# Optimization experiments

Hardware: AMD Instinct MI355X
Metric: run time of the kernel (lower is better)

## Reference

```python
import jax, jax.numpy as jnp
import numpy as np

B, T, I, H, C, S, V = 32, 64, 300, 168, 168, 512, 50257


def setup_inputs() -> dict:
    key = jax.random.key(0)
    ks = jax.random.split(key, 10)
    s = 0.05
    return {
        "x": jax.random.normal(ks[0], (B, T, I), jnp.float32),
        "context": jax.random.normal(ks[1], (B, S, C), jnp.float32),
        "context_lengths": jax.random.randint(ks[2], (B,), 1, S + 1),
        "W_ih": jax.random.normal(ks[3], (4 * H, I + C), jnp.float32) * s,
        "W_hh": jax.random.normal(ks[4], (4 * H, H), jnp.float32) * s,
        "b_ih": jnp.zeros((4 * H,), jnp.float32),
        "b_hh": jnp.zeros((4 * H,), jnp.float32),
        "att_Wx": jax.random.normal(ks[5], (H, H), jnp.float32) * s,
        "att_Ws": jax.random.normal(ks[6], (C, H), jnp.float32) * s,
        "att_b": jnp.zeros((H,), jnp.float32),
        "att_v": jax.random.normal(ks[7], (H,), jnp.float32) * s,
        "W_dec": jax.random.normal(ks[8], (V, H), jnp.float32) * s,
    }


def reference(x, context, context_lengths, W_ih, W_hh, b_ih, b_hh,
              att_Wx, att_Ws, att_b, att_v, W_dec):
    # x: (B, T, I); context: (B, S, C)
    b, t, _ = x.shape
    s_len = context.shape[1]
    h_dim = W_hh.shape[1]
    dtype = x.dtype

    # valid-position mask for attention over source context
    mask = jnp.arange(s_len)[None, :] < context_lengths[:, None]  # (B, S)
    # seq projection is time-invariant: precompute once outside the step loop
    seq_proj = jnp.einsum('bsc,ca->bsa', context, att_Ws)  # (B, S, H)

    h0 = jnp.zeros((b, h_dim), dtype)
    c0 = jnp.zeros((b, h_dim), dtype)

    def step(carry, x_t):
        h, c = carry
        # MLP (additive) attention: v . tanh(Wx h + Ws seq + b)
        e = jnp.einsum('bsa,a->bs',
                       jnp.tanh((h @ att_Wx)[:, None, :] + seq_proj + att_b),
                       att_v)  # (B, S)
        e = jnp.where(mask, e, jnp.asarray(-1e9, dtype))
        w = jax.nn.softmax(e, axis=-1)
        attn_ctx = jnp.einsum('bs,bsc->bc', w, context)  # (B, C)

        # concat input with attended context, single-layer LSTM cell
        rnn_in = jnp.concatenate([x_t, attn_ctx], axis=1)  # (B, I+C)
        gates = rnn_in @ W_ih.T + b_ih + h @ W_hh.T + b_hh  # (B, 4H)
        i_g, f_g, g_g, o_g = jnp.split(gates, 4, axis=1)    # torch ifgo order
        c_new = jax.nn.sigmoid(f_g) * c + jax.nn.sigmoid(i_g) * jnp.tanh(g_g)
        h_new = jax.nn.sigmoid(o_g) * jnp.tanh(c_new)

        dec = h_new @ W_dec.T  # (B, V), bias-free decode
        return (h_new, c_new), dec

    _, decs = jax.lax.scan(step, (h0, c0), jnp.swapaxes(x, 0, 1))  # (T, B, V)
    return jnp.swapaxes(decs, 0, 1)  # (B, T, V)
```

## Files before the change

### kernel.cpp

```cpp
#include <hip/hip_runtime.h>
#include <stdint.h>

#define BB 32
#define TT 64
#define ID 300
#define HH 168
#define SS 512
#define VV 50257
#define G4 672
#define IC 468
#define KP 192
#define NP2 50432
#define NJ 8
#define RPB 21
#define CPB 84
#define KK 336
#define WKP 88
#define EPAD 170
#define SBLK 64
#define LP 72

typedef float f32x4 __attribute__((ext_vector_type(4)));
typedef short bf16x8 __attribute__((ext_vector_type(8)));

__device__ __forceinline__ float bf2f(unsigned short u) {
  union { unsigned int i; float f; } v; v.i = ((unsigned int)u) << 16; return v.f;
}
__device__ __forceinline__ unsigned short f2bf(float f) {
  union { float f; unsigned int u; } v; v.f = f;
  unsigned int r = v.u + 0x7fffu + ((v.u >> 16) & 1u);
  return (unsigned short)(r >> 16);
}
__device__ __forceinline__ float rcpf(float x) { return __builtin_amdgcn_rcpf(x); }

#define NB_WDEC 4728
#define NB_TR   788
__global__ void k_prepall(const float* __restrict__ Wih, const float* __restrict__ Whh,
                          const float* __restrict__ attWx, const float* __restrict__ Wd,
                          float* __restrict__ WihxT, unsigned short* __restrict__ Wdb,
                          float* __restrict__ WgT, unsigned short* __restrict__ WxS,
                          unsigned int* __restrict__ flags, unsigned short* __restrict__ hall) {
  const int bid = blockIdx.x, tid = threadIdx.x;
  if (bid < NB_WDEC) {
    size_t e0 = ((size_t)bid * 256 + tid) * 8;
    int v = (int)(e0 / KP), k = (int)(e0 - (size_t)v * KP);
    unsigned short o[8];
    if (v < VV && k < HH) {
      const float* src = Wd + (size_t)v * HH + k;
      #pragma unroll
      for (int i = 0; i < 8; ++i) o[i] = f2bf(src[i]);
    } else {
      #pragma unroll
      for (int i = 0; i < 8; ++i) o[i] = 0;
    }
    *(uint4*)(Wdb + e0) = *(const uint4*)o;
    return;
  }
  if (bid < NB_WDEC + NB_TR) {
    int idx = (bid - NB_WDEC) * 256 + tid;
    if (idx < ID * G4) {
      int k = idx / G4, i = idx - k * G4;
      WihxT[idx] = Wih[(size_t)i * IC + k];
    }
    return;
  }
  int idx = (bid - NB_WDEC - NB_TR) * 256 + tid;
  const int T1 = NJ * KK * WKP;
  const int T2 = T1 + NJ * RPB * HH;
  const int T3 = T2 + 2 * BB * NJ * 64;
  const int T4 = T3 + BB * TT * (KP - HH);
  if (idx < T1) {
    int j = idx / (KK * WKP); int r = idx - j * (KK * WKP);
    int k = r / WKP, col = r - k * WKP;
    float w = 0.f;
    if (col < CPB) {
      int gt = col / RPB, rr = col - gt * RPB;
      int gcol = gt * HH + j * RPB + rr;
      w = (k < HH) ? Wih[(size_t)gcol * IC + ID + k] : Whh[(size_t)gcol * HH + (k - HH)];
    }
    WgT[idx] = w;
  } else if (idx < T2) {
    int r = idx - T1;
    WxS[r] = f2bf(attWx[r]);
  } else if (idx < T3) {
    flags[idx - T2] = 0u;
  } else if (idx < T4) {
    int r = idx - T3;
    int bt = r / (KP - HH), c = r - bt * (KP - HH);
    hall[(size_t)bt * KP + HH + c] = 0;
  }
}

__global__ void k_seqxp(const float* __restrict__ ctx, const float* __restrict__ Ws,
                        const float* __restrict__ x, const float* __restrict__ WihxT,
                        const float* __restrict__ bih, const float* __restrict__ bhh,
                        unsigned short* __restrict__ ETs, unsigned short* __restrict__ ctxb,
                        float* __restrict__ Xp) {
  __shared__ float sbuf[2688];
  const int tid = threadIdx.x;
  if (blockIdx.x < 1024) {
    const int b = blockIdx.x & 31;
    const int s0 = (blockIdx.x >> 5) * 16;
    for (int idx = tid; idx < 16 * HH; idx += 256) {
      float v = ctx[(size_t)(b * SS + s0) * HH + idx];
      sbuf[idx] = v;
      ctxb[(size_t)(b * SS + s0) * HH + idx] = f2bf(v);
    }
    __syncthreads();
    #pragma unroll
    for (int o = 0; o < 11; ++o) {
      int idx = o * 256 + tid;
      if (idx < 16 * HH) {
        int s = idx / HH, h = idx - s * HH;
        const float* cr = &sbuf[s * HH];
        float acc = 0.f;
        #pragma unroll 4
        for (int c = 0; c < HH; ++c) acc = fmaf(cr[c], Ws[c * HH + h], acc);
        ETs[(size_t)(b * SS + s0 + s) * HH + h] = f2bf(__expf(2.f * acc));
      }
    }
  } else {
    const int r = blockIdx.x - 1024;
    const int t0 = (r & 7) * 8;
    const int b = r >> 3;
    for (int idx = tid; idx < 8 * ID; idx += 256)
      sbuf[idx] = x[(size_t)(b * TT + t0) * ID + idx];
    __syncthreads();
    for (int i = tid; i < G4; i += 256) {
      float bias = bih[i] + bhh[i];
      float acc[8];
      #pragma unroll
      for (int tt = 0; tt < 8; ++tt) acc[tt] = bias;
      for (int k = 0; k < ID; ++k) {
        float w = WihxT[k * G4 + i];
        #pragma unroll
        for (int tt = 0; tt < 8; ++tt) acc[tt] += sbuf[tt * ID + k] * w;
      }
      #pragma unroll
      for (int tt = 0; tt < 8; ++tt)
        Xp[(size_t)(b * TT + t0 + tt) * G4 + i] = acc[tt];
    }
  }
}

__global__ __launch_bounds__(512, 1) void k_recur(
    const int* __restrict__ lens, const float* __restrict__ attb,
    const float* __restrict__ attv, const float* __restrict__ WgT,
    const unsigned short* __restrict__ WxS, const unsigned short* __restrict__ ETs,
    const unsigned short* __restrict__ ctxb, const float* __restrict__ Xp,
    float* __restrict__ Hbuf, float* __restrict__ Pbuf, float* __restrict__ APbuf,
    unsigned int* __restrict__ flags, unsigned short* __restrict__ hall) {
  const int b = blockIdx.x & 31;
  const int j = blockIdx.x >> 5;
  const int tid = threadIdx.x;

  __shared__ float WgL[KK][WKP];
  __shared__ unsigned short EL[SBLK][EPAD];
  __shared__ unsigned short WxL[RPB][HH];
  __shared__ float scratch[512];
  __shared__ float redH[504], redC[504];
  __shared__ float gE[HH], hsh[HH], abL[HH], vL[HH], attn[HH];
  __shared__ float esh[SBLK], hLoc[RPB], cLoc[RPB], wsum[8];
  __shared__ float sumv_s, bsum_s;

  {
    const f32x4* src = (const f32x4*)(WgT + (size_t)j * KK * WKP);
    f32x4* dst = (f32x4*)WgL;
    for (int i = tid; i < KK * WKP / 4; i += 512) dst[i] = src[i];
  }
  for (int i = tid; i < SBLK * HH; i += 512) {
    int s = i / HH, h = i - s * HH;
    EL[s][h] = ETs[((size_t)b * SS + j * SBLK + s) * HH + h];
  }
  for (int i = tid; i < RPB * HH; i += 512)
    ((unsigned short*)WxL)[i] = WxS[(size_t)j * RPB * HH + i];
  if (tid < HH) { abL[tid] = attb[tid]; vL[tid] = attv[tid]; }
  if (tid < RPB) cLoc[tid] = 0.f;
  __syncthreads();
  if (tid == 0) {
    float s = 0.f;
    for (int h = 0; h < HH; ++h) s += vL[h];
    sumv_s = s;
  }
  const int len = lens[b];
  const int sbase = j * SBLK;
  unsigned int* fB = flags + (size_t)(b * NJ) * 64;
  unsigned int* fA = flags + (size_t)BB * NJ * 64 + (size_t)(b * NJ) * 64;
  __syncthreads();

  for (int t = 0; t < TT; ++t) {
    float xpr0 = 0.f, xpr1 = 0.f, xpr2 = 0.f, xpr3 = 0.f;
    if (tid < RPB) {
      const float* xp = Xp + ((size_t)b * TT + t) * G4 + j * RPB + tid;
      xpr0 = xp[0]; xpr1 = xp[HH]; xpr2 = xp[2 * HH]; xpr3 = xp[3 * HH];
    }
    if (t > 0) {
      if (tid < NJ) {
        int g = 0;
        while (__hip_atomic_load(&fB[tid * 64], __ATOMIC_RELAXED,
                                 __HIP_MEMORY_SCOPE_AGENT) < (unsigned)t) {
          __builtin_amdgcn_s_sleep(2);
          if (++g > (1 << 27)) break;
        }
      }
      asm volatile("" ::: "memory");
      __syncthreads();
    }
    if (tid < HH) {
      float a = abL[tid];
      if (t > 0) {
        #pragma unroll
        for (int jj = 0; jj < NJ; ++jj)
          a += __hip_atomic_load(&APbuf[((size_t)b * NJ + jj) * HH + tid],
                                 __ATOMIC_RELAXED, __HIP_MEMORY_SCOPE_AGENT);
        hsh[tid] = __hip_atomic_load(&Hbuf[(size_t)b * HH + tid],
                                     __ATOMIC_RELAXED, __HIP_MEMORY_SCOPE_AGENT);
      } else {
        hsh[tid] = 0.f;
      }
      gE[tid] = __expf(2.f * a);
    }
    __syncthreads();
    {
      int w = tid >> 6, lane = tid & 63;
      int sl = w * 8 + (lane >> 3);
      int hg = lane & 7;
      const unsigned short* er = &EL[sl][hg * RPB];
      const int hb = hg * RPB;
      float ep = 0.f;
      #pragma unroll 7
      for (int i = 0; i < RPB; ++i)
        ep += vL[hb + i] * rcpf(fmaf(gE[hb + i], bf2f(er[i]), 1.f));
      ep += __shfl_xor(ep, 1); ep += __shfl_xor(ep, 2); ep += __shfl_xor(ep, 4);
      float eh = (sbase + sl < len) ? __expf(sumv_s - 2.f * ep) : 0.f;
      float ws = (hg == 0) ? eh : 0.f;
      ws += __shfl_xor(ws, 8); ws += __shfl_xor(ws, 16); ws += __shfl_xor(ws, 32);
      if (lane == 0) wsum[w] = ws;
      if (hg == 0) esh[sl] = eh;
    }
    __syncthreads();
    if (tid < 504) {
      int c = tid % HH, ch = tid / HH;
      const unsigned short* cb = ctxb + ((size_t)b * SS + sbase) * HH + c;
      float p = 0.f;
      for (int s = ch; s < SBLK; s += 3)
        p = fmaf(esh[s], bf2f(cb[(size_t)s * HH]), p);
      scratch[ch * HH + c] = p;
    } else if (tid == 504) {
      float bs = 0.f;
      #pragma unroll
      for (int w = 0; w < 8; ++w) bs += wsum[w];
      bsum_s = bs;
    }
    __syncthreads();
    if (tid < HH) {
      float p = scratch[tid] + scratch[HH + tid] + scratch[2 * HH + tid];
      __hip_atomic_store(&Pbuf[((size_t)b * NJ + j) * 176 + tid], p,
                         __ATOMIC_RELAXED, __HIP_MEMORY_SCOPE_AGENT);
    } else if (tid == HH) {
      __hip_atomic_store(&Pbuf[((size_t)b * NJ + j) * 176 + HH], bsum_s,
                         __ATOMIC_RELAXED, __HIP_MEMORY_SCOPE_AGENT);
    }
    __syncthreads();
    if (tid == 0) {
      asm volatile("s_waitcnt vmcnt(0)" ::: "memory");
      __hip_atomic_store(&fA[j * 64], (unsigned)(t + 1),
                         __ATOMIC_RELAXED, __HIP_MEMORY_SCOPE_AGENT);
    }
    if (tid < 504) {
      int col = tid % CPB, kc = tid / CPB;
      int k0 = HH + kc * 28;
      float acc = 0.f;
      #pragma unroll 7
      for (int i = 0; i < 28; ++i)
        acc = fmaf(WgL[k0 + i][col], hsh[kc * 28 + i], acc);
      redH[kc * CPB + col] = acc;
    }
    if (tid < NJ) {
      int g = 0;
      while (__hip_atomic_load(&fA[tid * 64], __ATOMIC_RELAXED,
                               __HIP_MEMORY_SCOPE_AGENT) < (unsigned)(t + 1)) {
        __builtin_amdgcn_s_sleep(2);
        if (++g > (1 << 27)) break;
      }
    }
    asm volatile("" ::: "memory");
    __syncthreads();
    if (tid < HH) {
      float s = 0.f, den = 0.f;
      #pragma unroll
      for (int jj = 0; jj < NJ; ++jj) {
        const float* pb = &Pbuf[((size_t)b * NJ + jj) * 176];
        s += __hip_atomic_load(&pb[tid], __ATOMIC_RELAXED, __HIP_MEMORY_SCOPE_AGENT);
        den += __hip_atomic_load(&pb[HH], __ATOMIC_RELAXED, __HIP_MEMORY_SCOPE_AGENT);
      }
      attn[tid] = s * rcpf(den);
    }
    __syncthreads();
    if (tid < 504) {
      int col = tid % CPB, kc = tid / CPB;
      int k0 = kc * 28;
      float acc = 0.f;
      #pragma unroll 7
      for (int i = 0; i < 28; ++i)
        acc = fmaf(WgL[k0 + i][col], attn[k0 + i], acc);
      redC[kc * CPB + col] = acc;
    }
    __syncthreads();
    if (tid < RPB) {
      float g0 = xpr0, g1 = xpr1, g2 = xpr2, g3 = xpr3;
      #pragma unroll
      for (int kc = 0; kc < 6; ++kc) {
        const float* rh = &redH[kc * CPB];
        const float* rc = &redC[kc * CPB];
        g0 += rh[tid] + rc[tid];
        g1 += rh[RPB + tid] + rc[RPB + tid];
        g2 += rh[2 * RPB + tid] + rc[2 * RPB + tid];
        g3 += rh[3 * RPB + tid] + rc[3 * RPB + tid];
      }
      float si = rcpf(1.f + __expf(-g0));
      float sf = rcpf(1.f + __expf(-g1));
      float tg = 1.f - 2.f * rcpf(1.f + __expf(2.f * g2));
      float so = rcpf(1.f + __expf(-g3));
      float cn = fmaf(sf, cLoc[tid], si * tg);
      float tc = 1.f - 2.f * rcpf(1.f + __expf(2.f * cn));
      float hn = so * tc;
      cLoc[tid] = cn; hLoc[tid] = hn;
      hall[((size_t)b * TT + t) * KP + j * RPB + tid] = f2bf(hn);
      __hip_atomic_store(&Hbuf[(size_t)b * HH + j * RPB + tid], hn,
                         __ATOMIC_RELAXED, __HIP_MEMORY_SCOPE_AGENT);
    }
    __syncthreads();
    if (tid < 504) {
      int col = tid % HH, ch = tid / HH;
      float acc = 0.f;
      #pragma unroll
      for (int r = ch * 7; r < ch * 7 + 7; ++r)
        acc = fmaf(hLoc[r], bf2f(WxL[r][col]), acc);
      scratch[ch * HH + col] = acc;
    }
    __syncthreads();
    if (tid < HH) {
      float a = scratch[tid] + scratch[HH + tid] + scratch[2 * HH + tid];
      __hip_atomic_store(&APbuf[((size_t)b * NJ + j) * HH + tid], a,
                         __ATOMIC_RELAXED, __HIP_MEMORY_SCOPE_AGENT);
    }
    __syncthreads();
    if (tid == 0) {
      asm volatile("s_waitcnt vmcnt(0)" ::: "memory");
      __hip_atomic_store(&fB[j * 64], (unsigned)(t + 1),
                         __ATOMIC_RELAXED, __HIP_MEMORY_SCOPE_AGENT);
    }
  }
}

__global__ __launch_bounds__(512, 1) void k_decode(const unsigned short* __restrict__ hallb,
                                                   const unsigned short* __restrict__ wdb,
                                                   float* __restrict__ out) {
  __shared__ __align__(16) unsigned short As[256 * LP];
  __shared__ __align__(16) unsigned short Bs[256 * LP];
  const int tid = threadIdx.x;
  const int n0 = blockIdx.x * 256, m0 = blockIdx.y * 256;
  const int lane = tid & 63, wid = tid >> 6;
  const int wm = wid >> 2, wn = wid & 3;
  const int lr = lane & 15, lk = lane >> 4;
  f32x4 acc[8][4];
  #pragma unroll
  for (int i = 0; i < 8; ++i)
    #pragma unroll
    for (int jj = 0; jj < 4; ++jj) acc[i][jj] = (f32x4)0.f;

  for (int k0 = 0; k0 < KP; k0 += 64) {
    if (k0) __syncthreads();
    #pragma unroll
    for (int i = 0; i < 4; ++i) {
      int flat = i * 512 + tid;
      int row = flat >> 3;
      int c8 = flat & 7;
      uint4 va = *(const uint4*)(hallb + (size_t)(m0 + row) * KP + k0 + c8 * 8);
      *(uint4*)&As[row * LP + c8 * 8] = va;
      uint4 vb = *(const uint4*)(wdb + (size_t)(n0 + row) * KP + k0 + c8 * 8);
      *(uint4*)&Bs[row * LP + c8 * 8] = vb;
    }
    __syncthreads();
    #pragma unroll
    for (int kk = 0; kk < 64; kk += 32) {
      bf16x8 af[8], bfr[4];
      #pragma unroll
      for (int mi = 0; mi < 8; ++mi)
        af[mi] = *(const bf16x8*)&As[(wm * 128 + mi * 16 + lr) * LP + kk + lk * 8];
      #pragma unroll
      for (int ni = 0; ni < 4; ++ni)
        bfr[ni] = *(const bf16x8*)&Bs[(wn * 64 + ni * 16 + lr) * LP + kk + lk * 8];
      #pragma unroll
      for (int mi = 0; mi < 8; ++mi)
        #pragma unroll
        for (int ni = 0; ni < 4; ++ni)
          acc[mi][ni] = __builtin_amdgcn_mfma_f32_16x16x32_bf16(
              af[mi], bfr[ni], acc[mi][ni], 0, 0, 0);
    }
  }
  #pragma unroll
  for (int mi = 0; mi < 8; ++mi)
    #pragma unroll
    for (int ni = 0; ni < 4; ++ni) {
      int col = n0 + wn * 64 + ni * 16 + lr;
      if (col < VV) {
        #pragma unroll
        for (int r = 0; r < 4; ++r) {
          int row = m0 + wm * 128 + mi * 16 + lk * 4 + r;
          out[(size_t)row * VV + col] = acc[mi][ni][r];
        }
      }
    }
}

extern "C" void kernel_launch(void* const* d_in, const int* in_sizes, int n_in,
                              void* d_out, int out_size, void* d_ws, size_t ws_size,
                              hipStream_t stream) {
  (void)in_sizes; (void)n_in; (void)out_size; (void)ws_size;
  const float* x     = (const float*)d_in[0];
  const float* ctx   = (const float*)d_in[1];
  const int*   lens  = (const int*)d_in[2];
  const float* Wih   = (const float*)d_in[3];
  const float* Whh   = (const float*)d_in[4];
  const float* bih   = (const float*)d_in[5];
  const float* bhh   = (const float*)d_in[6];
  const float* attWx = (const float*)d_in[7];
  const float* attWs = (const float*)d_in[8];
  const float* attb  = (const float*)d_in[9];
  const float* attv  = (const float*)d_in[10];
  const float* Wdec  = (const float*)d_in[11];
  float* out = (float*)d_out;

  char* base = (char*)d_ws;
  size_t off = 0;
  auto alloc = [&](size_t bytes) -> void* {
    off = (off + 255) & ~(size_t)255;
    void* p = base + off;
    off += bytes;
    return p;
  };
  unsigned short* ETs  = (unsigned short*)alloc((size_t)BB * SS * HH * 2);
  unsigned short* ctxb = (unsigned short*)alloc((size_t)BB * SS * HH * 2);
  float*          Xp   = (float*)alloc((size_t)BB * TT * G4 * 4);
  float*          WihxT= (float*)alloc((size_t)ID * G4 * 4);
  unsigned short* hall = (unsigned short*)alloc((size_t)BB * TT * KP * 2);
  unsigned short* Wdb  = (unsigned short*)alloc((size_t)NP2 * KP * 2);
  float*          WgT  = (float*)alloc((size_t)NJ * KK * WKP * 4);
  unsigned short* WxS  = (unsigned short*)alloc((size_t)NJ * RPB * HH * 2);
  float*          Hbuf = (float*)alloc((size_t)BB * HH * 4);
  float*          Pbuf = (float*)alloc((size_t)BB * NJ * 176 * 4);
  float*          APbuf= (float*)alloc((size_t)BB * NJ * HH * 4);
  unsigned int*   flags= (unsigned int*)alloc((size_t)2 * BB * NJ * 64 * 4);

  {
    const int TOTP = NJ * KK * WKP + NJ * RPB * HH + 2 * BB * NJ * 64 + BB * TT * (KP - HH);
    const int NBP = (TOTP + 255) / 256;
    k_prepall<<<dim3(NB_WDEC + NB_TR + NBP), dim3(256), 0, stream>>>(
        Wih, Whh, attWx, Wdec, WihxT, Wdb, WgT, WxS, flags, hall);
  }
  k_seqxp<<<dim3(1024 + 256), dim3(256), 0, stream>>>(ctx, attWs, x, WihxT,
                                                      bih, bhh, ETs, ctxb, Xp);
  {
    const int* a0 = lens; const float* a1 = attb; const float* a2 = attv;
    const float* a3 = WgT; const unsigned short* a4 = WxS;
    const unsigned short* a5 = ETs; const unsigned short* a6 = ctxb;
    const float* a7 = Xp; float* a8 = Hbuf; float* a9 = Pbuf; float* a10 = APbuf;
    unsigned int* a11 = flags; unsigned short* a12 = hall;
    void* args[] = { &a0, &a1, &a2, &a3, &a4, &a5, &a6, &a7, &a8, &a9, &a10, &a11, &a12 };
    hipLaunchCooperativeKernel((void*)k_recur, dim3(BB * NJ), dim3(512), args, 0, stream);
  }
  k_decode<<<dim3(NP2 / 256, (BB * TT) / 256), dim3(512), 0, stream>>>(hall, Wdb, out);
}
```

Baseline: 814.1 us.

## Replace flag-based inter-block sync with tagged 64-bit value slots

The separate flag words and their barrier/fence sequence in the cooperative recurrence kernel are replaced by 64-bit slots that pack each float with its timestep tag. Consumers spin directly on the data they need until every tag reaches the expected step. This removes the s_waitcnt-plus-flag-store round trip and several __syncthreads per step, which sit on the serial recurrence's critical path. In exchange, 168 threads per block now poll many global words each iteration instead of 8 threads polling flags, which raises memory traffic and contention.

```diff
diff --git a/kernel.cpp b/kernel.cpp
--- a/kernel.cpp
+++ b/kernel.cpp
@@ -19,9 +19,11 @@
 #define EPAD 170
 #define SBLK 64
 #define LP 72
+#define LSLOT 192
 
 typedef float f32x4 __attribute__((ext_vector_type(4)));
 typedef short bf16x8 __attribute__((ext_vector_type(8)));
+typedef unsigned long long u64;
 
 __device__ __forceinline__ float bf2f(unsigned short u) {
   union { unsigned int i; float f; } v; v.i = ((unsigned int)u) << 16; return v.f;
@@ -32,6 +34,20 @@
   return (unsigned short)(r >> 16);
 }
 __device__ __forceinline__ float rcpf(float x) { return __builtin_amdgcn_rcpf(x); }
+__device__ __forceinline__ u64 packft(float f, unsigned tag) {
+  union { float f; unsigned u; } v; v.f = f;
+  return ((u64)tag << 32) | (u64)v.u;
+}
+__device__ __forceinline__ float lo_f(u64 x) {
+  union { unsigned u; float f; } v; v.u = (unsigned)x; return v.f;
+}
+__device__ __forceinline__ unsigned hi_u(u64 x) { return (unsigned)(x >> 32); }
+__device__ __forceinline__ void postv(u64* p, u64 v) {
+  __hip_atomic_store(p, v, __ATOMIC_RELAXED, __HIP_MEMORY_SCOPE_AGENT);
+}
+__device__ __forceinline__ u64 loadv(const u64* p) {
+  return __hip_atomic_load(p, __ATOMIC_RELAXED, __HIP_MEMORY_SCOPE_AGENT);
+}
 
 #define NB_WDEC 4728
 #define NB_TR   788
@@ -39,7 +55,8 @@
                           const float* __restrict__ attWx, const float* __restrict__ Wd,
                           float* __restrict__ WihxT, unsigned short* __restrict__ Wdb,
                           float* __restrict__ WgT, unsigned short* __restrict__ WxS,
-                          unsigned int* __restrict__ flags, unsigned short* __restrict__ hall) {
+                          u64* __restrict__ Abuf, u64* __restrict__ Pbuf,
+                          unsigned short* __restrict__ hall) {
   const int bid = blockIdx.x, tid = threadIdx.x;
   if (bid < NB_WDEC) {
     size_t e0 = ((size_t)bid * 256 + tid) * 8;
@@ -67,7 +84,8 @@
   int idx = (bid - NB_WDEC - NB_TR) * 256 + tid;
   const int T1 = NJ * KK * WKP;
   const int T2 = T1 + NJ * RPB * HH;
-  const int T3 = T2 + 2 * BB * NJ * 64;
+  const int ZH = BB * NJ * LSLOT;
+  const int T3 = T2 + 2 * ZH;
   const int T4 = T3 + BB * TT * (KP - HH);
   if (idx < T1) {
     int j = idx / (KK * WKP); int r = idx - j * (KK * WKP);
@@ -83,7 +101,9 @@
     int r = idx - T1;
     WxS[r] = f2bf(attWx[r]);
   } else if (idx < T3) {
-    flags[idx - T2] = 0u;
+    int r = idx - T2;
+    if (r < ZH) Abuf[r] = 0ull;
+    else        Pbuf[r - ZH] = 0ull;
   } else if (idx < T4) {
     int r = idx - T3;
     int bt = r / (KP - HH), c = r - bt * (KP - HH);
@@ -148,8 +168,8 @@
     const float* __restrict__ attv, const float* __restrict__ WgT,
     const unsigned short* __restrict__ WxS, const unsigned short* __restrict__ ETs,
     const unsigned short* __restrict__ ctxb, const float* __restrict__ Xp,
-    float* __restrict__ Hbuf, float* __restrict__ Pbuf, float* __restrict__ APbuf,
-    unsigned int* __restrict__ flags, unsigned short* __restrict__ hall) {
+    u64* __restrict__ Abuf, u64* __restrict__ Pbuf,
+    unsigned short* __restrict__ hall) {
   const int b = blockIdx.x & 31;
   const int j = blockIdx.x >> 5;
   const int tid = threadIdx.x;
@@ -184,8 +204,8 @@
   }
   const int len = lens[b];
   const int sbase = j * SBLK;
-  unsigned int* fB = flags + (size_t)(b * NJ) * 64;
-  unsigned int* fA = flags + (size_t)BB * NJ * 64 + (size_t)(b * NJ) * 64;
+  u64* Amine = Abuf + (size_t)(b * NJ + j) * LSLOT;
+  u64* Pmine = Pbuf + (size_t)(b * NJ + j) * LSLOT;
   __syncthreads();
 
   for (int t = 0; t < TT; ++t) {
@@ -194,31 +214,31 @@
       const float* xp = Xp + ((size_t)b * TT + t) * G4 + j * RPB + tid;
       xpr0 = xp[0]; xpr1 = xp[HH]; xpr2 = xp[2 * HH]; xpr3 = xp[3 * HH];
     }
-    if (t > 0) {
-      if (tid < NJ) {
+    if (tid < HH) {
+      float a = abL[tid], hv = 0.f;
+      if (t > 0) {
+        const unsigned want = (unsigned)t;
+        const int jh = tid / RPB, hr = tid - jh * RPB;
+        u64 va[9];
         int g = 0;
-        while (__hip_atomic_load(&fB[tid * 64], __ATOMIC_RELAXED,
-                                 __HIP_MEMORY_SCOPE_AGENT) < (unsigned)t) {
-          __builtin_amdgcn_s_sleep(2);
-          if (++g > (1 << 27)) break;
+        for (;;) {
+          #pragma unroll
+          for (int jj = 0; jj < NJ; ++jj)
+            va[jj] = loadv(&Abuf[(size_t)(b * NJ + jj) * LSLOT + tid]);
+          va[8] = loadv(&Abuf[(size_t)(b * NJ + jh) * LSLOT + HH + hr]);
+          bool ok = true;
+          #pragma unroll
+          for (int q = 0; q < 9; ++q) ok &= (hi_u(va[q]) >= want);
+          if (ok) break;
+          __builtin_amdgcn_s_sleep(1);
+          if (++g > (1 << 24)) break;
         }
-      }
-      asm volatile("" ::: "memory");
-      __syncthreads();
-    }
-    if (tid < HH) {
-      float a = abL[tid];
-      if (t > 0) {
-        #pragma unroll
-        for (int jj = 0; jj < NJ; ++jj)
-          a += __hip_atomic_load(&APbuf[((size_t)b * NJ + jj) * HH + tid],
-                                 __ATOMIC_RELAXED, __HIP_MEMORY_SCOPE_AGENT);
-        hsh[tid] = __hip_atomic_load(&Hbuf[(size_t)b * HH + tid],
-                                     __ATOMIC_RELAXED, __HIP_MEMORY_SCOPE_AGENT);
-      } else {
-        hsh[tid] = 0.f;
+        #pragma unroll
+        for (int jj = 0; jj < NJ; ++jj) a += lo_f(va[jj]);
+        hv = lo_f(va[8]);
       }
       gE[tid] = __expf(2.f * a);
+      hsh[tid] = hv;
     }
     __syncthreads();
     {
@@ -255,17 +275,9 @@
     __syncthreads();
     if (tid < HH) {
       float p = scratch[tid] + scratch[HH + tid] + scratch[2 * HH + tid];
-      __hip_atomic_store(&Pbuf[((size_t)b * NJ + j) * 176 + tid], p,
-                         __ATOMIC_RELAXED, __HIP_MEMORY_SCOPE_AGENT);
+      postv(&Pmine[tid], packft(p, (unsigned)(t + 1)));
     } else if (tid == HH) {
-      __hip_atomic_store(&Pbuf[((size_t)b * NJ + j) * 176 + HH], bsum_s,
-                         __ATOMIC_RELAXED, __HIP_MEMORY_SCOPE_AGENT);
-    }
-    __syncthreads();
-    if (tid == 0) {
-      asm volatile("s_waitcnt vmcnt(0)" ::: "memory");
-      __hip_atomic_store(&fA[j * 64], (unsigned)(t + 1),
-                         __ATOMIC_RELAXED, __HIP_MEMORY_SCOPE_AGENT);
+      postv(&Pmine[HH], packft(bsum_s, (unsigned)(t + 1)));
     }
     if (tid < 504) {
       int col = tid % CPB, kc = tid / CPB;
@@ -276,24 +288,27 @@
         acc = fmaf(WgL[k0 + i][col], hsh[kc * 28 + i], acc);
       redH[kc * CPB + col] = acc;
     }
-    if (tid < NJ) {
+    if (tid < HH) {
+      const unsigned want = (unsigned)(t + 1);
+      u64 pv[NJ], bv[NJ];
       int g = 0;
-      while (__hip_atomic_load(&fA[tid * 64], __ATOMIC_RELAXED,
-                               __HIP_MEMORY_SCOPE_AGENT) < (unsigned)(t + 1)) {
-        __builtin_amdgcn_s_sleep(2);
-        if (++g > (1 << 27)) break;
-      }
-    }
-    asm volatile("" ::: "memory");
-    __syncthreads();
-    if (tid < HH) {
+      for (;;) {
+        #pragma unroll
+        for (int jj = 0; jj < NJ; ++jj) {
+          const u64* pb = Pbuf + (size_t)(b * NJ + jj) * LSLOT;
+          pv[jj] = loadv(&pb[tid]);
+          bv[jj] = loadv(&pb[HH]);
+        }
+        bool ok = true;
+        #pragma unroll
+        for (int jj = 0; jj < NJ; ++jj) ok &= (hi_u(pv[jj]) >= want) & (hi_u(bv[jj]) >= want);
+        if (ok) break;
+        __builtin_amdgcn_s_sleep(1);
+        if (++g > (1 << 24)) break;
+      }
       float s = 0.f, den = 0.f;
       #pragma unroll
-      for (int jj = 0; jj < NJ; ++jj) {
-        const float* pb = &Pbuf[((size_t)b * NJ + jj) * 176];
-        s += __hip_atomic_load(&pb[tid], __ATOMIC_RELAXED, __HIP_MEMORY_SCOPE_AGENT);
-        den += __hip_atomic_load(&pb[HH], __ATOMIC_RELAXED, __HIP_MEMORY_SCOPE_AGENT);
-      }
+      for (int jj = 0; jj < NJ; ++jj) { s += lo_f(pv[jj]); den += lo_f(bv[jj]); }
       attn[tid] = s * rcpf(den);
     }
     __syncthreads();
@@ -327,8 +342,6 @@
       float hn = so * tc;
       cLoc[tid] = cn; hLoc[tid] = hn;
       hall[((size_t)b * TT + t) * KP + j * RPB + tid] = f2bf(hn);
-      __hip_atomic_store(&Hbuf[(size_t)b * HH + j * RPB + tid], hn,
-                         __ATOMIC_RELAXED, __HIP_MEMORY_SCOPE_AGENT);
     }
     __syncthreads();
     if (tid < 504) {
@@ -342,14 +355,9 @@
     __syncthreads();
     if (tid < HH) {
       float a = scratch[tid] + scratch[HH + tid] + scratch[2 * HH + tid];
-      __hip_atomic_store(&APbuf[((size_t)b * NJ + j) * HH + tid], a,
-                         __ATOMIC_RELAXED, __HIP_MEMORY_SCOPE_AGENT);
-    }
-    __syncthreads();
-    if (tid == 0) {
-      asm volatile("s_waitcnt vmcnt(0)" ::: "memory");
-      __hip_atomic_store(&fB[j * 64], (unsigned)(t + 1),
-                         __ATOMIC_RELAXED, __HIP_MEMORY_SCOPE_AGENT);
+      postv(&Amine[tid], packft(a, (unsigned)(t + 1)));
+    } else if (tid < HH + RPB) {
+      postv(&Amine[tid], packft(hLoc[tid - HH], (unsigned)(t + 1)));
     }
   }
 }
@@ -449,16 +457,14 @@
   unsigned short* Wdb  = (unsigned short*)alloc((size_t)NP2 * KP * 2);
   float*          WgT  = (float*)alloc((size_t)NJ * KK * WKP * 4);
   unsigned short* WxS  = (unsigned short*)alloc((size_t)NJ * RPB * HH * 2);
-  float*          Hbuf = (float*)alloc((size_t)BB * HH * 4);
-  float*          Pbuf = (float*)alloc((size_t)BB * NJ * 176 * 4);
-  float*          APbuf= (float*)alloc((size_t)BB * NJ * HH * 4);
-  unsigned int*   flags= (unsigned int*)alloc((size_t)2 * BB * NJ * 64 * 4);
+  u64*            Abuf = (u64*)alloc((size_t)BB * NJ * LSLOT * 8);
+  u64*            Pbuf = (u64*)alloc((size_t)BB * NJ * LSLOT * 8);
 
   {
-    const int TOTP = NJ * KK * WKP + NJ * RPB * HH + 2 * BB * NJ * 64 + BB * TT * (KP - HH);
+    const int TOTP = NJ * KK * WKP + NJ * RPB * HH + 2 * BB * NJ * LSLOT + BB * TT * (KP - HH);
     const int NBP = (TOTP + 255) / 256;
     k_prepall<<<dim3(NB_WDEC + NB_TR + NBP), dim3(256), 0, stream>>>(
-        Wih, Whh, attWx, Wdec, WihxT, Wdb, WgT, WxS, flags, hall);
+        Wih, Whh, attWx, Wdec, WihxT, Wdb, WgT, WxS, Abuf, Pbuf, hall);
   }
   k_seqxp<<<dim3(1024 + 256), dim3(256), 0, stream>>>(ctx, attWs, x, WihxT,
                                                       bih, bhh, ETs, ctxb, Xp);
@@ -466,9 +472,9 @@
     const int* a0 = lens; const float* a1 = attb; const float* a2 = attv;
     const float* a3 = WgT; const unsigned short* a4 = WxS;
     const unsigned short* a5 = ETs; const unsigned short* a6 = ctxb;
-    const float* a7 = Xp; float* a8 = Hbuf; float* a9 = Pbuf; float* a10 = APbuf;
-    unsigned int* a11 = flags; unsigned short* a12 = hall;
-    void* args[] = { &a0, &a1, &a2, &a3, &a4, &a5, &a6, &a7, &a8, &a9, &a10, &a11, &a12 };
+    const float* a7 = Xp; u64* a8 = Abuf; u64* a9 = Pbuf;
+    unsigned short* a10 = hall;
+    void* args[] = { &a0, &a1, &a2, &a3, &a4, &a5, &a6, &a7, &a8, &a9, &a10 };
     hipLaunchCooperativeKernel((void*)k_recur, dim3(BB * NJ), dim3(512), args, 0, stream);
   }
   k_decode<<<dim3(NP2 / 256, (BB * TT) / 256), dim3(512), 0, stream>>>(hall, Wdb, out);
```

New measurement: 757.2 us. -7.0%, faster.
